# Optimization experiments

Hardware: AMD Instinct MI355X
Metric: run time of the kernel (lower is better)

The kernel has to match this reference:

```python
import jax, jax.numpy as jnp
import numpy as np

V_WORD, V_CHAR = 50000, 128
EMB, CEMB, FILT, K = 300, 32, 4, 3
HID = 512
T, B, W = 128, 64, 16
OUT = 20
CCH = CEMB * FILT  # 128 conv output channels
LSTM_IN = EMB + CCH  # 428


def setup_inputs() -> dict:
    key = jax.random.key(0)
    ks = jax.random.split(key, 20)
    s = 0.1  # matches init_weights std
    inp = {
        "words": jax.random.randint(ks[0], (T, B), 0, V_WORD),
        "chars": jax.random.randint(ks[1], (B, T, W), 0, V_CHAR),
        "emb_W": s * jax.random.normal(ks[2], (V_WORD, EMB), jnp.float32),
        "char_emb_W": s * jax.random.normal(ks[3], (V_CHAR, CEMB), jnp.float32),
        "conv_W": s * jax.random.normal(ks[4], (CCH, 1, K), jnp.float32),
        "conv_b": s * jax.random.normal(ks[5], (CCH,), jnp.float32),
        "Wih_f": s * jax.random.normal(ks[6], (4 * HID, LSTM_IN), jnp.float32),
        "Whh_f": s * jax.random.normal(ks[7], (4 * HID, HID), jnp.float32),
        "bih_f": s * jax.random.normal(ks[8], (4 * HID,), jnp.float32),
        "bhh_f": s * jax.random.normal(ks[9], (4 * HID,), jnp.float32),
        "Wih_b": s * jax.random.normal(ks[10], (4 * HID, LSTM_IN), jnp.float32),
        "Whh_b": s * jax.random.normal(ks[11], (4 * HID, HID), jnp.float32),
        "bih_b": s * jax.random.normal(ks[12], (4 * HID,), jnp.float32),
        "bhh_b": s * jax.random.normal(ks[13], (4 * HID,), jnp.float32),
        "fc_W": s * jax.random.normal(ks[14], (OUT, 2 * HID), jnp.float32),
        "fc_b": s * jax.random.normal(ks[15], (OUT,), jnp.float32),
    }
    return inp


def _lstm_dir(x, Wih, Whh, bih, bhh):
    # x: [T, B, I] -> hs: [T, B, H]; PyTorch gate order i, f, g, o
    H = Whh.shape[1]
    b = bih + bhh
    xW = jnp.einsum("tbi,gi->tbg", x, Wih) + b  # precompute input projections

    def step(carry, xt):
        h, c = carry
        z = xt + h @ Whh.T  # [B, 4H]
        i, f, g, o = jnp.split(z, 4, axis=-1)
        c = jax.nn.sigmoid(f) * c + jax.nn.sigmoid(i) * jnp.tanh(g)
        h = jax.nn.sigmoid(o) * jnp.tanh(c)
        return (h, c), h

    h0 = jnp.zeros((x.shape[1], H), x.dtype)
    _, hs = jax.lax.scan(step, (h0, h0), xW)
    return hs


def reference(words, chars, emb_W, char_emb_W, conv_W, conv_b,
              Wih_f, Whh_f, bih_f, bhh_f, Wih_b, Whh_b, bih_b, bhh_b,
              fc_W, fc_b):
    # word embeddings: [T, B, EMB]
    emb_out = emb_W[words]
    # char embeddings: [B, T, W, CEMB] -> batched depthwise-grouped conv over all words at once
    ce = char_emb_W[chars]
    x = ce.reshape(B * T, W, CEMB).transpose(0, 2, 1)  # [B*T, CEMB, W]
    conv = jax.lax.conv_general_dilated(
        x, conv_W, window_strides=(1,), padding="VALID",
        feature_group_count=CEMB,
        dimension_numbers=("NCH", "OIH", "NCH"))  # [B*T, CCH, W-K+1]
    conv = conv + conv_b[None, :, None]
    char_cnn_max = conv.max(axis=2).reshape(B, T, CCH)  # [B, T, CCH]
    char_cnn_p = char_cnn_max.transpose(1, 0, 2)  # [T, B, CCH]
    feat = jnp.concatenate([emb_out, char_cnn_p], axis=2)  # [T, B, 428]
    h_f = _lstm_dir(feat, Wih_f, Whh_f, bih_f, bhh_f)
    h_b = _lstm_dir(feat[::-1], Wih_b, Whh_b, bih_b, bhh_b)[::-1]
    lstm_out = jnp.concatenate([h_f, h_b], axis=2)  # [T, B, 2H]
    return lstm_out @ fc_W.T + fc_b  # [T, B, OUT]
```

## Files before the change

### kernel.cpp

```cpp
#include <hip/hip_runtime.h>
#include <hip/hip_bf16.h>

#define TT 128
#define BATCH 64
#define WCH 16
#define CEMB 32
#define CCH 128
#define HID 512
#define GATES 2048
#define INF_ 428
#define KP 448
#define NOUT 20

typedef float f32x4 __attribute__((ext_vector_type(4)));
typedef __bf16 b8v __attribute__((ext_vector_type(8)));
typedef unsigned int u32x2 __attribute__((ext_vector_type(2)));
typedef unsigned int u32x4 __attribute__((ext_vector_type(4)));
typedef __hip_bfloat16 bf16;

__device__ __forceinline__ float sigm(float x){ return 1.f/(1.f+__expf(-x)); }
__device__ __forceinline__ float tanh_(float x){ float e=__expf(2.f*x); return (e-1.f)/(e+1.f); }

__global__ void k_feat(const int* __restrict__ words, const int* __restrict__ chars,
                       const float* __restrict__ embW, const float* __restrict__ cembW,
                       const float* __restrict__ convW, const float* __restrict__ convb,
                       bf16* __restrict__ featb) {
  int r = blockIdx.x;
  int t = r >> 6, b = r & 63;
  int tid = threadIdx.x;
  int wi = words[t*BATCH + b];
  const float* src = embW + (size_t)wi * 300;
  bf16* dst = featb + (size_t)r * KP;
  for (int k = tid; k < 300; k += 128) dst[k] = __float2bfloat16(src[k]);
  if (tid < KP - INF_) dst[INF_ + tid] = __float2bfloat16(0.f);
  int cc = tid, g = cc >> 2;
  const int* ch = chars + ((size_t)b*TT + t)*WCH;
  float ce[WCH];
  #pragma unroll
  for (int w = 0; w < WCH; ++w) ce[w] = cembW[ch[w]*CEMB + g];
  float w0 = convW[cc*3], w1 = convW[cc*3+1], w2 = convW[cc*3+2];
  float m = -1e30f;
  #pragma unroll
  for (int p = 0; p < WCH-2; ++p) m = fmaxf(m, ce[p]*w0 + ce[p+1]*w1 + ce[p+2]*w2);
  dst[300 + cc] = __float2bfloat16(m + convb[cc]);
}

__global__ void k_pack(const float* __restrict__ WihF, const float* __restrict__ WhhF,
                       const float* __restrict__ bihF, const float* __restrict__ bhhF,
                       const float* __restrict__ WihB, const float* __restrict__ WhhB,
                       const float* __restrict__ bihB, const float* __restrict__ bhhB,
                       bf16* __restrict__ Wihp, bf16* __restrict__ Whhp, float* __restrict__ bsum) {
  size_t tid0 = (size_t)blockIdx.x*blockDim.x + threadIdx.x;
  size_t nthr = (size_t)gridDim.x*blockDim.x;
  for (size_t idx = tid0; idx < (size_t)2*GATES*HID; idx += nthr) {
    int k = idx & (HID-1);
    int p = (idx >> 9) & (GATES-1);
    int d = (int)(idx >> 20);
    int j = ((p>>5)<<3) | (p&7);
    int tau = (p>>3)&3;
    const float* Whh = d ? WhhB : WhhF;
    Whhp[idx] = __float2bfloat16(Whh[(size_t)(tau*HID + j)*HID + k]);
  }
  for (size_t idx = tid0; idx < (size_t)2*GATES*KP; idx += nthr) {
    int k = (int)(idx % KP);
    size_t rest = idx / KP;
    int p = (int)(rest & (GATES-1));
    int d = (int)(rest >> 11);
    int j = ((p>>5)<<3) | (p&7);
    int tau = (p>>3)&3;
    const float* Wih = d ? WihB : WihF;
    float v = (k < INF_) ? Wih[(size_t)(tau*HID + j)*INF_ + k] : 0.f;
    Wihp[idx] = __float2bfloat16(v);
  }
  for (size_t idx = tid0; idx < (size_t)2*GATES; idx += nthr) {
    int p = (int)(idx & (GATES-1));
    int d = (int)(idx >> 11);
    int j = ((p>>5)<<3) | (p&7);
    int tau = (p>>3)&3;
    int gg = tau*HID + j;
    bsum[idx] = d ? (bihB[gg]+bhhB[gg]) : (bihF[gg]+bhhF[gg]);
  }
}

__global__ __launch_bounds__(256) void k_gemm(const bf16* __restrict__ Wihp,
      const bf16* __restrict__ featb, const float* __restrict__ bsum,
      bf16* __restrict__ xW) {
  __shared__ short As[128][72];
  __shared__ short Bs[128][72];
  int m0 = (blockIdx.x & 31) << 7;
  int n0 = (blockIdx.x >> 5) << 7;
  int tid = threadIdx.x;
  int lane = tid & 63;
  int wid = tid >> 6;
  int wr = wid >> 1, wc = wid & 1;
  int lm = lane & 15, kg = lane >> 4;
  f32x4 acc[4][4] = {};
  for (int k0 = 0; k0 < KP; k0 += 64) {
    #pragma unroll
    for (int c = 0; c < 4; ++c) {
      int ch = tid + c*256;
      int row = ch >> 3, k8 = (ch & 7) << 3;
      *(b8v*)&As[row][k8] = *(const b8v*)&Wihp[(size_t)(m0+row)*KP + k0 + k8];
      *(b8v*)&Bs[row][k8] = *(const b8v*)&featb[(size_t)(n0+row)*KP + k0 + k8];
    }
    __syncthreads();
    #pragma unroll
    for (int ks = 0; ks < 2; ++ks) {
      b8v a[4], bb[4];
      #pragma unroll
      for (int i = 0; i < 4; ++i) a[i]  = *(const b8v*)&As[wr*64 + i*16 + lm][ks*32 + kg*8];
      #pragma unroll
      for (int i = 0; i < 4; ++i) bb[i] = *(const b8v*)&Bs[wc*64 + i*16 + lm][ks*32 + kg*8];
      #pragma unroll
      for (int mi = 0; mi < 4; ++mi)
        #pragma unroll
        for (int ni = 0; ni < 4; ++ni)
          acc[mi][ni] = __builtin_amdgcn_mfma_f32_16x16x32_bf16(a[mi], bb[ni], acc[mi][ni], 0, 0, 0);
    }
    __syncthreads();
  }
  #pragma unroll
  for (int mi = 0; mi < 4; ++mi) {
    #pragma unroll
    for (int ni = 0; ni < 4; ++ni) {
      int r = n0 + wc*64 + ni*16 + lm;
      int t = r >> 6, b = r & 63;
      #pragma unroll
      for (int reg = 0; reg < 4; ++reg) {
        int G = m0 + wr*64 + mi*16 + kg*4 + reg;
        int d = G >> 11, p = G & (GATES-1);
        int jt_ = p >> 5, pp = p & 31;
        int noff = ((pp>>2)&3)*8 + (pp>>4)*4 + (pp&3);
        float v = acc[mi][ni][reg] + bsum[G];
        xW[(((size_t)t*2 + d)*64 + jt_)*2048 + b*32 + noff] = __float2bfloat16(v);
      }
    }
  }
}

__global__ __launch_bounds__(256, 1) void k_persist(
    const bf16* __restrict__ Whhp, const bf16* __restrict__ xW,
    bf16* __restrict__ hs, unsigned* __restrict__ flags) {
  const int tid = threadIdx.x;
  const int widx = tid >> 6;
  const int wid = blockIdx.x*4 + widx;
  const int lane = tid & 63;
  const int dir = wid >> 8;
  const int btile = (wid >> 6) & 3;
  const int jt = wid & 63;
  const int grp = blockIdx.x >> 4;
  const int wv = ((blockIdx.x & 15) << 2) | widx;
  const int b0 = btile << 4, pbase = jt << 5, jbase = jt << 3;
  const int col = lane & 15, kg = lane >> 4;

  __shared__ __align__(16) bf16 hlds[16*512];

  b8v wa0[16], wa1[16];
  {
    const bf16* wp = Whhp + (size_t)dir*GATES*HID;
    #pragma unroll
    for (int ks = 0; ks < 16; ++ks) {
      wa0[ks] = *(const b8v*)&wp[(size_t)(pbase + col)*HID + ks*32 + kg*8];
      wa1[ks] = *(const b8v*)&wp[(size_t)(pbase + 16 + col)*HID + ks*32 + kg*8];
    }
    #pragma unroll
    for (int ks = 0; ks < 16; ++ks) {
      asm("" : "+v"(wa0[ks]));
      asm("" : "+v"(wa1[ks]));
    }
  }
  const bf16* const xwbase = xW + (size_t)jt*2048 + (b0 + col)*32 + kg*8;
  b8v nx;
  {
    const int t0 = dir ? TT-1 : 0;
    nx = *(const b8v*)(xwbase + (size_t)(t0*2 + dir)*64*2048);
  }
  f32x4 creg = {0.f, 0.f, 0.f, 0.f};

  for (int step = 0; step < TT; ++step) {
    const int tcur = dir ? (TT-1-step) : step;
    f32x4 acc0, acc1;
    #pragma unroll
    for (int r = 0; r < 4; ++r) { acc0[r] = (float)nx[r]; acc1[r] = (float)nx[r+4]; }
    if (step > 0) {
      if (widx == 0) {
        const unsigned* fp = flags + (((size_t)(step-1)*8 + grp) << 6) + lane;
        for (;;) {
          unsigned v;
          asm volatile("global_load_dword %0, %1, off sc0 sc1\n\ts_waitcnt vmcnt(0)"
                       : "=v"(v) : "v"(fp) : "memory");
          if (__all(v == (unsigned)step)) break;
          __builtin_amdgcn_s_sleep(1);
        }
      }
      __syncthreads();
      const int tprev = dir ? tcur+1 : tcur-1;
      const bf16* hbase = hs + (((size_t)dir*TT + tprev)*BATCH + b0)*HID;
      u32x4 tmp0, tmp1, tmp2, tmp3;
      {
        const bf16* a0 = hbase + (size_t)tid*8;
        const bf16* a1 = a0 + 2048;
        const bf16* a2 = a0 + 4096;
        const bf16* a3 = a0 + 6144;
        asm volatile("global_load_dwordx4 %0, %1, off sc0 sc1" : "=v"(tmp0) : "v"(a0) : "memory");
        asm volatile("global_load_dwordx4 %0, %1, off sc0 sc1" : "=v"(tmp1) : "v"(a1) : "memory");
        asm volatile("global_load_dwordx4 %0, %1, off sc0 sc1" : "=v"(tmp2) : "v"(a2) : "memory");
        asm volatile("global_load_dwordx4 %0, %1, off sc0 sc1" : "=v"(tmp3) : "v"(a3) : "memory");
      }
      asm volatile("s_waitcnt vmcnt(0)" ::: "memory");
      __builtin_amdgcn_sched_barrier(0);
      #pragma unroll
      for (int p = 0; p < 4; ++p) {
        int c = p*256 + tid;
        int b = c >> 6, j8 = c & 63;
        int slot = j8 ^ (b & 7);
        u32x4 val = (p==0) ? tmp0 : (p==1) ? tmp1 : (p==2) ? tmp2 : tmp3;
        *(u32x4*)&hlds[b*512 + slot*8] = val;
      }
      __syncthreads();
      #pragma unroll
      for (int ks = 0; ks < 16; ++ks) {
        int slotr = (ks*4 + kg) ^ (col & 7);
        b8v bfrag = *(const b8v*)&hlds[col*512 + slotr*8];
        acc0 = __builtin_amdgcn_mfma_f32_16x16x32_bf16(wa0[ks], bfrag, acc0, 0, 0, 0);
        acc1 = __builtin_amdgcn_mfma_f32_16x16x32_bf16(wa1[ks], bfrag, acc1, 0, 0, 0);
      }
    }
    f32x4 fsh, osh;
    #pragma unroll
    for (int r = 0; r < 4; ++r) {
      fsh[r] = __shfl_xor(acc0[r], 32);
      osh[r] = __shfl_xor(acc1[r], 32);
    }
    if (lane < 32) {
      unsigned us[4];
      #pragma unroll
      for (int r = 0; r < 4; ++r) {
        float zi = acc0[r], zf = fsh[r], zg = acc1[r], zo = osh[r];
        float co = (step > 0) ? creg[r] : 0.f;
        float cn = sigm(zf)*co + sigm(zi)*tanh_(zg);
        creg[r] = cn;
        us[r] = (unsigned)__builtin_bit_cast(unsigned short, __float2bfloat16(sigm(zo)*tanh_(cn)));
      }
      u32x2 pk; pk.x = us[0] | (us[1] << 16); pk.y = us[2] | (us[3] << 16);
      bf16* hpw = hs + (((size_t)dir*TT + tcur)*BATCH + b0 + col)*HID + jbase + kg*4;
      asm volatile("global_store_dwordx2 %0, %1, off sc0 sc1"
                   :: "v"(hpw), "v"(pk) : "memory");
    }
    if (step + 1 < TT) {
      asm volatile("s_waitcnt vmcnt(0)" ::: "memory");
      if (lane == 0) {
        unsigned* fw = flags + (((size_t)step*8 + grp) << 6) + wv;
        unsigned val = (unsigned)(step + 1);
        asm volatile("global_store_dword %0, %1, off sc0 sc1"
                     :: "v"(fw), "v"(val) : "memory");
      }
      const int tnext = dir ? tcur-1 : tcur+1;
      nx = *(const b8v*)(xwbase + (size_t)(tnext*2 + dir)*64*2048);
    }
  }
}

__global__ __launch_bounds__(256) void k_fc(const bf16* __restrict__ hs,
                     const float* __restrict__ fcW,
                     const float* __restrict__ fcb, float* __restrict__ out) {
  int t = blockIdx.x;
  for (int item = threadIdx.x; item < BATCH*NOUT; item += 256) {
    const int b = item / NOUT, o = item - b*NOUT;
    const b8v* hf8 = (const b8v*)(hs + ((size_t)t*BATCH + b)*HID);
    const b8v* hb8 = (const b8v*)(hs + (((size_t)TT + t)*BATCH + b)*HID);
    const float4* w4 = (const float4*)(fcW + (size_t)o*2*HID);
    float s = fcb[o];
    #pragma unroll 4
    for (int k = 0; k < 64; ++k) {
      b8v hv = hf8[k];
      float4 wa = w4[2*k], wb = w4[2*k+1];
      s += (float)hv[0]*wa.x + (float)hv[1]*wa.y + (float)hv[2]*wa.z + (float)hv[3]*wa.w
         + (float)hv[4]*wb.x + (float)hv[5]*wb.y + (float)hv[6]*wb.z + (float)hv[7]*wb.w;
    }
    #pragma unroll 4
    for (int k = 0; k < 64; ++k) {
      b8v hv = hb8[k];
      float4 wa = w4[128 + 2*k], wb = w4[129 + 2*k];
      s += (float)hv[0]*wa.x + (float)hv[1]*wa.y + (float)hv[2]*wa.z + (float)hv[3]*wa.w
         + (float)hv[4]*wb.x + (float)hv[5]*wb.y + (float)hv[6]*wb.z + (float)hv[7]*wb.w;
    }
    out[((size_t)t*BATCH + b)*NOUT + o] = s;
  }
}

extern "C" void kernel_launch(void* const* d_in, const int* in_sizes, int n_in,
                              void* d_out, int out_size, void* d_ws, size_t ws_size,
                              hipStream_t stream) {
  const int* words = (const int*)d_in[0];
  const int* chars = (const int*)d_in[1];
  const float* embW = (const float*)d_in[2];
  const float* cembW = (const float*)d_in[3];
  const float* convW = (const float*)d_in[4];
  const float* convb = (const float*)d_in[5];
  const float* WihF = (const float*)d_in[6];
  const float* WhhF = (const float*)d_in[7];
  const float* bihF = (const float*)d_in[8];
  const float* bhhF = (const float*)d_in[9];
  const float* WihB = (const float*)d_in[10];
  const float* WhhB = (const float*)d_in[11];
  const float* bihB = (const float*)d_in[12];
  const float* bhhB = (const float*)d_in[13];
  const float* fcW = (const float*)d_in[14];
  const float* fcb = (const float*)d_in[15];
  float* out = (float*)d_out;

  char* ws = (char*)d_ws;
  size_t off = 0;
  bf16* xW    = (bf16*)(ws + off); off += (size_t)TT*2*GATES*BATCH*2;
  bf16* hsbuf = (bf16*)(ws + off); off += (size_t)2*TT*BATCH*HID*2;
  bf16* featb = (bf16*)(ws + off); off += (size_t)TT*BATCH*KP*2;
  bf16* Wihp  = (bf16*)(ws + off); off += (size_t)2*GATES*KP*2;
  bf16* Whhp  = (bf16*)(ws + off); off += (size_t)2*GATES*HID*2;
  float* bsum = (float*)(ws + off); off += (size_t)2*GATES*4;
  unsigned* flags = (unsigned*)(ws + off); off += (size_t)TT*8*64*4;
  if (off > ws_size) return;

  hipMemsetAsync(flags, 0, (size_t)TT*8*64*4, stream);
  k_feat<<<TT*BATCH, 128, 0, stream>>>(words, chars, embW, cembW, convW, convb, featb);
  k_pack<<<2048, 256, 0, stream>>>(WihF, WhhF, bihF, bhhF, WihB, WhhB, bihB, bhhB,
                                   Wihp, Whhp, bsum);
  k_gemm<<<2048, 256, 0, stream>>>(Wihp, featb, bsum, xW);

  void* kargs[] = { (void*)&Whhp, (void*)&xW, (void*)&hsbuf, (void*)&flags };
  hipLaunchCooperativeKernel((const void*)k_persist, dim3(128), dim3(256),
                             kargs, 0, stream);
  k_fc<<<TT, 256, 0, stream>>>(hsbuf, fcW, fcb, out);
}
```

Measured before the change: 670.7 us.

## Spin per-wave on flags, split MFMA chains, keep weights in AGPRs

In the persistent LSTM kernel, every wave now polls the step flags itself, with no sleep. This removes the wave-0 poll followed by a block-wide barrier. The recurrent matmul is split into two independent MFMA accumulation chains (even and odd k-slices) that are summed at the end, which shortens the dependency chain. The recurrent weights are pinned to accumulation registers through asm constraints, and the next-step xW prefetch is issued before the waitcnt so it overlaps the flag store. The costs are more polling traffic, a risk of unsupported AGPR operand use, and the need to move weights from AGPRs back to VGPRs for each MFMA.

```diff
diff --git a/kernel.cpp b/kernel.cpp
--- a/kernel.cpp
+++ b/kernel.cpp
@@ -155,18 +155,18 @@
 
   __shared__ __align__(16) bf16 hlds[16*512];
 
-  b8v wa0[16], wa1[16];
+  u32x4 wq0[16], wq1[16];
   {
     const bf16* wp = Whhp + (size_t)dir*GATES*HID;
     #pragma unroll
     for (int ks = 0; ks < 16; ++ks) {
-      wa0[ks] = *(const b8v*)&wp[(size_t)(pbase + col)*HID + ks*32 + kg*8];
-      wa1[ks] = *(const b8v*)&wp[(size_t)(pbase + 16 + col)*HID + ks*32 + kg*8];
+      wq0[ks] = *(const u32x4*)&wp[(size_t)(pbase + col)*HID + ks*32 + kg*8];
+      wq1[ks] = *(const u32x4*)&wp[(size_t)(pbase + 16 + col)*HID + ks*32 + kg*8];
     }
     #pragma unroll
     for (int ks = 0; ks < 16; ++ks) {
-      asm("" : "+v"(wa0[ks]));
-      asm("" : "+v"(wa1[ks]));
+      asm("" : "+a"(wq0[ks]));
+      asm("" : "+a"(wq1[ks]));
     }
   }
   const bf16* const xwbase = xW + (size_t)jt*2048 + (b0 + col)*32 + kg*8;
@@ -180,20 +180,15 @@
   for (int step = 0; step < TT; ++step) {
     const int tcur = dir ? (TT-1-step) : step;
     f32x4 acc0, acc1;
-    #pragma unroll
-    for (int r = 0; r < 4; ++r) { acc0[r] = (float)nx[r]; acc1[r] = (float)nx[r+4]; }
     if (step > 0) {
-      if (widx == 0) {
+      {
         const unsigned* fp = flags + (((size_t)(step-1)*8 + grp) << 6) + lane;
-        for (;;) {
-          unsigned v;
+        unsigned v;
+        do {
           asm volatile("global_load_dword %0, %1, off sc0 sc1\n\ts_waitcnt vmcnt(0)"
                        : "=v"(v) : "v"(fp) : "memory");
-          if (__all(v == (unsigned)step)) break;
-          __builtin_amdgcn_s_sleep(1);
-        }
-      }
-      __syncthreads();
+        } while (!__all(v == (unsigned)step));
+      }
       const int tprev = dir ? tcur+1 : tcur-1;
       const bf16* hbase = hs + (((size_t)dir*TT + tprev)*BATCH + b0)*HID;
       u32x4 tmp0, tmp1, tmp2, tmp3;
@@ -218,13 +213,25 @@
         *(u32x4*)&hlds[b*512 + slot*8] = val;
       }
       __syncthreads();
-      #pragma unroll
-      for (int ks = 0; ks < 16; ++ks) {
-        int slotr = (ks*4 + kg) ^ (col & 7);
-        b8v bfrag = *(const b8v*)&hlds[col*512 + slotr*8];
-        acc0 = __builtin_amdgcn_mfma_f32_16x16x32_bf16(wa0[ks], bfrag, acc0, 0, 0, 0);
-        acc1 = __builtin_amdgcn_mfma_f32_16x16x32_bf16(wa1[ks], bfrag, acc1, 0, 0, 0);
-      }
+      f32x4 z0, z1, y0 = {0.f,0.f,0.f,0.f}, y1 = {0.f,0.f,0.f,0.f};
+      #pragma unroll
+      for (int r = 0; r < 4; ++r) { z0[r] = (float)nx[r]; z1[r] = (float)nx[r+4]; }
+      #pragma unroll
+      for (int ks = 0; ks < 16; ks += 2) {
+        int se = (ks*4 + kg) ^ (col & 7);
+        int so = ((ks+1)*4 + kg) ^ (col & 7);
+        b8v fe = *(const b8v*)&hlds[col*512 + se*8];
+        b8v fo = *(const b8v*)&hlds[col*512 + so*8];
+        z0 = __builtin_amdgcn_mfma_f32_16x16x32_bf16(__builtin_bit_cast(b8v, wq0[ks]),   fe, z0, 0, 0, 0);
+        z1 = __builtin_amdgcn_mfma_f32_16x16x32_bf16(__builtin_bit_cast(b8v, wq1[ks]),   fe, z1, 0, 0, 0);
+        y0 = __builtin_amdgcn_mfma_f32_16x16x32_bf16(__builtin_bit_cast(b8v, wq0[ks+1]), fo, y0, 0, 0, 0);
+        y1 = __builtin_amdgcn_mfma_f32_16x16x32_bf16(__builtin_bit_cast(b8v, wq1[ks+1]), fo, y1, 0, 0, 0);
+      }
+      acc0 = z0 + y0;
+      acc1 = z1 + y1;
+    } else {
+      #pragma unroll
+      for (int r = 0; r < 4; ++r) { acc0[r] = (float)nx[r]; acc1[r] = (float)nx[r+4]; }
     }
     f32x4 fsh, osh;
     #pragma unroll
@@ -248,6 +255,8 @@
                    :: "v"(hpw), "v"(pk) : "memory");
     }
     if (step + 1 < TT) {
+      const int tnext = dir ? tcur-1 : tcur+1;
+      nx = *(const b8v*)(xwbase + (size_t)(tnext*2 + dir)*64*2048);
       asm volatile("s_waitcnt vmcnt(0)" ::: "memory");
       if (lane == 0) {
         unsigned* fw = flags + (((size_t)step*8 + grp) << 6) + wv;
@@ -255,8 +264,6 @@
         asm volatile("global_store_dword %0, %1, off sc0 sc1"
                      :: "v"(fw), "v"(val) : "memory");
       }
-      const int tnext = dir ? tcur-1 : tcur+1;
-      nx = *(const b8v*)(xwbase + (size_t)(tnext*2 + dir)*64*2048);
     }
   }
 }
```

After: 923.8 us. 37.7% more time.
